# Performance work log

Measured on AMD Instinct MI355X. Metric: run time of the kernel, lower is better.

Reference implementation:

```python
import jax, jax.numpy as jnp
import numpy as np

# Mamba2 hyperparams (mamba_ssm defaults given __init__ args)
D_MODEL = 512
FF = 2048
D_STATE = 128
D_CONV = 4
EXPAND = 2
D_INNER = EXPAND * D_MODEL          # 1024
HEADDIM = 64
NHEADS = D_INNER // HEADDIM         # 16
NGROUPS = 1
CONV_DIM = D_INNER + 2 * NGROUPS * D_STATE       # 1280
D_IN_PROJ = 2 * D_INNER + 2 * NGROUPS * D_STATE + NHEADS  # 2320
CHUNK = 128
EPS = 1e-5


def setup_inputs() -> dict:
    key = jax.random.key(0)
    ks = jax.random.split(key, 16)
    B, S = 8, 2048
    s = 0.02
    dt_init = jax.random.uniform(ks[4], (NHEADS,), minval=0.001, maxval=0.1)
    return {
        # forward args (dropout treated as eval / identity)
        "tgt": jax.random.normal(ks[0], (B, S, D_MODEL), jnp.float32),
        "memory": jax.random.normal(ks[1], (B, 256, D_MODEL), jnp.float32),
        "spatial_shapes": jnp.array([[16, 16]], jnp.int32),
        "level_start_index": jnp.array([0], jnp.int32),
        "valid_ratios": jnp.ones((B, 1, 2), jnp.float32),
        # Mamba2 params
        "in_proj_w": jax.random.normal(ks[2], (D_IN_PROJ, D_MODEL), jnp.float32) * s,
        "conv_w": jax.random.normal(ks[3], (CONV_DIM, D_CONV), jnp.float32) * s,
        "conv_b": jnp.zeros((CONV_DIM,), jnp.float32),
        "dt_bias": jnp.log(jnp.expm1(dt_init)),  # inverse softplus of dt_init
        "A_log": jnp.log(jax.random.uniform(ks[5], (NHEADS,), minval=1.0, maxval=16.0)),
        "D_head": jnp.ones((NHEADS,), jnp.float32),
        "norm_w": jnp.ones((D_INNER,), jnp.float32),
        "out_proj_w": jax.random.normal(ks[6], (D_MODEL, D_INNER), jnp.float32) * s,
        # LayerNorms + FFN
        "norm1_w": jnp.ones((D_MODEL,)), "norm1_b": jnp.zeros((D_MODEL,)),
        "w1": jax.random.normal(ks[7], (FF, D_MODEL), jnp.float32) * s,
        "b1": jnp.zeros((FF,)),
        "w2": jax.random.normal(ks[8], (D_MODEL, FF), jnp.float32) * s,
        "b2": jnp.zeros((D_MODEL,)),
        "norm3_w": jnp.ones((D_MODEL,)), "norm3_b": jnp.zeros((D_MODEL,)),
    }


def _layer_norm(x, w, b):
    m = jnp.mean(x, -1, keepdims=True)
    v = jnp.mean((x - m) ** 2, -1, keepdims=True)
    return (x - m) * jax.lax.rsqrt(v + EPS) * w + b


def _ssd(x, dt, A, Bm, Cm):
    # chunked selective-scan (SSD). x:(b,s,h,p) dt:(b,s,h) A:(h,) Bm,Cm:(b,s,n)
    b, s, h, p = x.shape
    n = Bm.shape[-1]
    c, l = s // CHUNK, CHUNK
    x = x.reshape(b, c, l, h, p)
    dt = dt.reshape(b, c, l, h)
    Bm = Bm.reshape(b, c, l, n)
    Cm = Cm.reshape(b, c, l, n)
    a_cs = jnp.cumsum(dt * A, axis=2)                 # (b,c,l,h) cumulative log-decay
    ac = a_cs.transpose(0, 1, 3, 2)                   # (b,c,h,l)
    mask = jnp.tril(jnp.ones((l, l), bool))
    Lmat = jnp.exp(jnp.where(mask, ac[..., :, None] - ac[..., None, :], -jnp.inf))
    # intra-chunk (causal) contribution
    Y_diag = jnp.einsum('bcin,bcjn,bchij,bcjh,bcjhp->bcihp', Cm, Bm, Lmat, dt, x)
    # per-chunk final states
    decay_end = jnp.exp(a_cs[:, :, -1:, :] - a_cs)    # (b,c,l,h)
    states = jnp.einsum('bcln,bclh,bclh,bclhp->bchpn', Bm, decay_end, dt, x)
    chunk_decay = jnp.exp(a_cs[:, :, -1, :])          # (b,c,h)
    def step(h0, inp):
        cd, st = inp
        return cd[:, :, None, None] * h0 + st, h0
    h_init = jnp.zeros((b, h, p, n), x.dtype)
    _, prev = jax.lax.scan(step, h_init,
                           (chunk_decay.transpose(1, 0, 2),
                            states.transpose(1, 0, 2, 3, 4)))
    prev = prev.transpose(1, 0, 2, 3, 4)              # (b,c,h,p,n) state at chunk start
    Y_off = jnp.einsum('bcln,bchpn,bclh->bclhp', Cm, prev, jnp.exp(a_cs))
    return (Y_diag + Y_off).reshape(b, s, h, p)


def _mamba2(u, in_proj_w, conv_w, conv_b, dt_bias, A_log, D_head, norm_w, out_proj_w):
    Bb, S, _ = u.shape
    zxbcdt = u @ in_proj_w.T                          # (b,s,2320)
    z, xBC, dt = jnp.split(zxbcdt, [D_INNER, D_INNER + CONV_DIM], axis=-1)
    # causal depthwise conv1d + silu
    xp = jnp.pad(xBC, ((0, 0), (D_CONV - 1, 0), (0, 0)))
    conv = sum(xp[:, k:k + S, :] * conv_w[:, k] for k in range(D_CONV)) + conv_b
    xBC = jax.nn.silu(conv)
    x, Bm, Cm = jnp.split(xBC, [D_INNER, D_INNER + NGROUPS * D_STATE], axis=-1)
    dt = jax.nn.softplus(dt + dt_bias)                # (b,s,h)
    A = -jnp.exp(A_log)                               # (h,)
    x = x.reshape(Bb, S, NHEADS, HEADDIM)
    y = _ssd(x, dt, A, Bm, Cm) + D_head[None, None, :, None] * x
    y = y.reshape(Bb, S, D_INNER)
    # gated RMSNorm: rmsnorm(y * silu(z)) * w
    y = y * jax.nn.silu(z)
    y = y * jax.lax.rsqrt(jnp.mean(y * y, -1, keepdims=True) + EPS) * norm_w
    return y @ out_proj_w.T


def reference(tgt, memory, spatial_shapes, level_start_index, valid_ratios,
              in_proj_w, conv_w, conv_b, dt_bias, A_log, D_head, norm_w, out_proj_w,
              norm1_w, norm1_b, w1, b1, w2, b2, norm3_w, norm3_b):
    t2 = _mamba2(tgt, in_proj_w, conv_w, conv_b, dt_bias, A_log, D_head, norm_w, out_proj_w)
    t = _layer_norm(tgt + t2, norm1_w, norm1_b)
    ff = jax.nn.gelu(t @ w1.T + b1, approximate=False) @ w2.T + b2
    return _layer_norm(t + ff, norm3_w, norm3_b)
```

## Files before the change

### kernel.cpp

```cpp
#include <hip/hip_runtime.h>
#include <hip/hip_bf16.h>
#include <math.h>


namespace {
constexpr int BB = 8;
constexpr int S = 2048;
constexpr int DM = 512;
constexpr int DIP = 2320;
constexpr int DIPP = 2432;
constexpr int DI = 1024;
constexpr int CDIM = 1280;
constexpr int NH = 16;
constexpr int HD = 64;
constexpr int DSTATE = 128;
constexpr int CH = 128;
constexpr int NC = S / CH;
constexpr int FF = 2048;
constexpr float EPS = 1e-5f;
constexpr int LP = 132;
}

using bf16_t = __hip_bfloat16;
typedef __attribute__((ext_vector_type(8))) short short8;
typedef __attribute__((ext_vector_type(4))) float f32x4;

__device__ __forceinline__ float gelu_exact(float x) {
    return 0.5f * x * (1.0f + erff(x * 0.7071067811865476f));
}
__device__ __forceinline__ unsigned short f2bfu(float f) {
    bf16_t b = __float2bfloat16(f);
    return *(unsigned short*)&b;
}
__device__ __forceinline__ float bfu2f(unsigned short u) {
    union { unsigned int i; float f; } v; v.i = (unsigned)u << 16; return v.f;
}

__device__ __forceinline__ void block_sum2(float& a, float& b) {
    #pragma unroll
    for (int o = 32; o > 0; o >>= 1) {
        a += __shfl_down(a, o, 64);
        b += __shfl_down(b, o, 64);
    }
    __shared__ float sa[4], sb[4];
    int w = threadIdx.x >> 6;
    if ((threadIdx.x & 63) == 0) { sa[w] = a; sb[w] = b; }
    __syncthreads();
    a = sa[0] + sa[1] + sa[2] + sa[3];
    b = sb[0] + sb[1] + sb[2] + sb[3];
}

template <int BM, int ACT, bool HASBIAS, bool OUTBF>
__global__ __launch_bounds__(256)
void mfma_gemm(const bf16_t* __restrict__ A, const bf16_t* __restrict__ W,
               const float* __restrict__ bias, void* __restrict__ Cout,
               int N, int K, int lda, int ldw, int ldc,
               long batchA, long batchW, long batchC)
{
    A += (long)blockIdx.z * batchA;
    W += (long)blockIdx.z * batchW;
    constexpr int ACH = BM / 64;
    constexpr int NJ = (BM == 128) ? 4 : 2;
    __shared__ bf16_t As[2][BM * 32];
    __shared__ bf16_t Ws[2][4096];
    const int tid = threadIdx.x;
    const int lane = tid & 63;
    const int wave = tid >> 6;
    const long bm = (long)blockIdx.y * BM;
    const int bn = blockIdx.x * 128;

    const int rA = tid & (BM - 1);
    const int qA = tid / BM;
    const int rW = tid & 127;
    const int qW = tid >> 7;
    const bf16_t* Ag = A + (bm + rA) * (long)lda + qA * 8;
    const bf16_t* Wg = W + ((long)bn + rW) * (long)ldw + qW * 8;
    const int laoff0 = (qA * BM + rA) * 8;
    const int laoff1 = ((qA + 2) * BM + rA) * 8;
    const int lwoff0 = (qW * 128 + rW) * 8;
    const int lwoff1 = ((qW + 2) * 128 + rW) * 8;

    const int kq = lane >> 4;
    const int lr = lane & 15;
    const int wm = (BM == 128) ? (wave & 1) * 64 : 0;
    const int wn = (BM == 128) ? (wave >> 1) * 64 : wave * 32;

    f32x4 acc[4][NJ];
    #pragma unroll
    for (int i = 0; i < 4; i++)
        #pragma unroll
        for (int j = 0; j < NJ; j++) acc[i][j] = (f32x4){0.f, 0.f, 0.f, 0.f};

    short8 ra0, ra1, rw0, rw1;
    ra0 = *(const short8*)Ag;
    if (ACH == 2) ra1 = *(const short8*)(Ag + 16);
    rw0 = *(const short8*)Wg;
    rw1 = *(const short8*)(Wg + 16);
    *(short8*)&As[0][laoff0] = ra0;
    if (ACH == 2) *(short8*)&As[0][laoff1] = ra1;
    *(short8*)&Ws[0][lwoff0] = rw0;
    *(short8*)&Ws[0][lwoff1] = rw1;

    const int nt = K / 32;
    for (int t = 0; t < nt; t++) {
        const int cur = t & 1, nxt = cur ^ 1;
        if (t + 1 < nt) {
            const int ko = (t + 1) * 32;
            ra0 = *(const short8*)(Ag + ko);
            if (ACH == 2) ra1 = *(const short8*)(Ag + ko + 16);
            rw0 = *(const short8*)(Wg + ko);
            rw1 = *(const short8*)(Wg + ko + 16);
        }
        __syncthreads();
        short8 af[4], bfr[NJ];
        #pragma unroll
        for (int i = 0; i < 4; i++)
            af[i] = *(const short8*)&As[cur][(kq * BM + wm + i * 16 + lr) * 8];
        #pragma unroll
        for (int j = 0; j < NJ; j++)
            bfr[j] = *(const short8*)&Ws[cur][(kq * 128 + wn + j * 16 + lr) * 8];
        #pragma unroll
        for (int i = 0; i < 4; i++)
            #pragma unroll
            for (int j = 0; j < NJ; j++)
                acc[i][j] = __builtin_amdgcn_mfma_f32_16x16x32_bf16(af[i], bfr[j], acc[i][j], 0, 0, 0);
        if (t + 1 < nt) {
            *(short8*)&As[nxt][laoff0] = ra0;
            if (ACH == 2) *(short8*)&As[nxt][laoff1] = ra1;
            *(short8*)&Ws[nxt][lwoff0] = rw0;
            *(short8*)&Ws[nxt][lwoff1] = rw1;
        }
    }

    #pragma unroll
    for (int i = 0; i < 4; i++) {
        #pragma unroll
        for (int j = 0; j < NJ; j++) {
            int col = bn + wn + j * 16 + lr;
            if (col < N) {
                float bv = HASBIAS ? bias[col] : 0.f;
                #pragma unroll
                for (int r = 0; r < 4; r++) {
                    long row = bm + wm + i * 16 + kq * 4 + r;
                    float v = acc[i][j][r] + bv;
                    if (ACT == 1) v = gelu_exact(v);
                    if (OUTBF) ((bf16_t*)Cout)[row * (long)ldc + col + blockIdx.z * batchC] = __float2bfloat16(v);
                    else       ((float*)Cout)[row * (long)ldc + col + blockIdx.z * batchC] = v;
                }
            }
        }
    }
}

template <int ACT, bool HASBIAS>
__global__ __launch_bounds__(256)
void gemm_kernel(const float* __restrict__ A, const float* __restrict__ W,
                 const float* __restrict__ bias, float* __restrict__ C,
                 int M, int N, int K, int lda, int ldw, int ldc,
                 long batchA, long batchW, long batchC)
{
    A += (long)blockIdx.z * batchA;
    W += (long)blockIdx.z * batchW;
    C += (long)blockIdx.z * batchC;
    __shared__ __align__(16) float Asm[16][68];
    __shared__ __align__(16) float Wsm[16][68];
    const int tid = threadIdx.x;
    const int bm = blockIdx.y * 64;
    const int bn = blockIdx.x * 64;
    const int tm = (tid & 15) * 4;
    const int tn = (tid >> 4) * 4;
    const int lr = tid >> 2;
    const int lk = (tid & 3) * 4;
    const float* Ap = A + (long)(bm + lr) * lda + lk;
    const float* Wp = W + (long)(bn + lr) * ldw + lk;
    const bool wv_ok = (bn + lr) < N;
    float acc[4][4];
    #pragma unroll
    for (int i = 0; i < 4; i++)
        #pragma unroll
        for (int j = 0; j < 4; j++) acc[i][j] = 0.f;

    for (int k0 = 0; k0 < K; k0 += 16) {
        float4 av = *(const float4*)(Ap + k0);
        float4 wv = wv_ok ? *(const float4*)(Wp + k0) : make_float4(0.f, 0.f, 0.f, 0.f);
        Asm[lk + 0][lr] = av.x; Asm[lk + 1][lr] = av.y;
        Asm[lk + 2][lr] = av.z; Asm[lk + 3][lr] = av.w;
        Wsm[lk + 0][lr] = wv.x; Wsm[lk + 1][lr] = wv.y;
        Wsm[lk + 2][lr] = wv.z; Wsm[lk + 3][lr] = wv.w;
        __syncthreads();
        #pragma unroll
        for (int k = 0; k < 16; k++) {
            float4 a = *(const float4*)&Asm[k][tm];
            float4 w = *(const float4*)&Wsm[k][tn];
            acc[0][0] += a.x * w.x; acc[0][1] += a.x * w.y; acc[0][2] += a.x * w.z; acc[0][3] += a.x * w.w;
            acc[1][0] += a.y * w.x; acc[1][1] += a.y * w.y; acc[1][2] += a.y * w.z; acc[1][3] += a.y * w.w;
            acc[2][0] += a.z * w.x; acc[2][1] += a.z * w.y; acc[2][2] += a.z * w.z; acc[2][3] += a.z * w.w;
            acc[3][0] += a.w * w.x; acc[3][1] += a.w * w.y; acc[3][2] += a.w * w.z; acc[3][3] += a.w * w.w;
        }
        __syncthreads();
    }
    #pragma unroll
    for (int i = 0; i < 4; i++) {
        long row = bm + tm + i;
        #pragma unroll
        for (int j = 0; j < 4; j++) {
            int col = bn + tn + j;
            if (col < N) {
                float v = acc[i][j];
                if (HASBIAS) v += bias[col];
                if (ACT == 1) v = gelu_exact(v);
                C[row * ldc + col] = v;
            }
        }
    }
}

__global__ __launch_bounds__(256)
void cvt_bf16(const float* __restrict__ s, bf16_t* __restrict__ d, long n)
{
    long i = ((long)blockIdx.x * 256 + threadIdx.x) * 4;
    if (i >= n) return;
    float4 v = *(const float4*)(s + i);
    d[i + 0] = __float2bfloat16(v.x);
    d[i + 1] = __float2bfloat16(v.y);
    d[i + 2] = __float2bfloat16(v.z);
    d[i + 3] = __float2bfloat16(v.w);
}

__global__ __launch_bounds__(256)
void cvt_bf16_pad(const float* __restrict__ s, bf16_t* __restrict__ d,
                  int rows_src, long total, int cols)
{
    long i = (long)blockIdx.x * 256 + threadIdx.x;
    if (i >= total) return;
    long r = i / cols;
    d[i] = __float2bfloat16(r < rows_src ? s[i] : 0.f);
}

__global__ __launch_bounds__(256)
void conv_silu4(const bf16_t* __restrict__ zx, const float* __restrict__ cw,
                const float* __restrict__ cb, bf16_t* __restrict__ xBC, long count4)
{
    long i4 = (long)blockIdx.x * 256 + threadIdx.x;
    if (i4 >= count4) return;
    long idx = i4 * 4;
    int c = (int)(idx % CDIM);
    long t = idx / CDIM;
    int s = (int)(t % S);
    float v0 = cb[c], v1 = cb[c + 1], v2 = cb[c + 2], v3 = cb[c + 3];
    #pragma unroll
    for (int k = 0; k < 4; k++) {
        int sp = s + k - 3;
        if (sp >= 0) {
            const bf16_t* p = zx + (t + k - 3) * DIP + DI + c;
            unsigned long long u = *(const unsigned long long*)p;
            v0 += bfu2f((unsigned short)(u      )) * cw[(c + 0) * 4 + k];
            v1 += bfu2f((unsigned short)(u >> 16)) * cw[(c + 1) * 4 + k];
            v2 += bfu2f((unsigned short)(u >> 32)) * cw[(c + 2) * 4 + k];
            v3 += bfu2f((unsigned short)(u >> 48)) * cw[(c + 3) * 4 + k];
        }
    }
    v0 = v0 / (1.f + __expf(-v0));
    v1 = v1 / (1.f + __expf(-v1));
    v2 = v2 / (1.f + __expf(-v2));
    v3 = v3 / (1.f + __expf(-v3));
    unsigned long long o = (unsigned long long)f2bfu(v0)
                         | ((unsigned long long)f2bfu(v1) << 16)
                         | ((unsigned long long)f2bfu(v2) << 32)
                         | ((unsigned long long)f2bfu(v3) << 48);
    *(unsigned long long*)&xBC[idx] = o;
}

__global__ __launch_bounds__(256)
void dt_kernel(const float* __restrict__ raw, const float* __restrict__ dt_bias,
               float* __restrict__ dts, long count)
{
    long idx = (long)blockIdx.x * 256 + threadIdx.x;
    if (idx >= count) return;
    float x = raw[idx] + dt_bias[idx & 15];
    dts[idx] = (x > 20.f) ? x : log1pf(__expf(x));
}

__global__ __launch_bounds__(256)
void ssd_states(const bf16_t* __restrict__ xBC, const float* __restrict__ dts,
                const float* __restrict__ A_log,
                float* __restrict__ st, float* __restrict__ acs_all,
                float* __restrict__ cdlog)
{
    const int bid = blockIdx.x;
    const int nh = bid & 1;
    const int h = (bid >> 1) & 15;
    const int c = (bid >> 5) & 15;
    const int b = bid >> 9;
    const int sbid = (b * NC + c) * NH + h;
    const int tid = threadIdx.x;
    const int lane = tid & 63;
    const int wave = tid >> 6;
    __shared__ float dtv[128];
    __shared__ float acs[128];
    __shared__ float wj[128];
    __shared__ bf16_t XT[64 * LP];
    __shared__ bf16_t BwT[64 * LP];
    const long t0 = (long)b * S + (long)c * CH;
    const float Ah = -__expf(A_log[h]);

    if (tid < 128) {
        float d = dts[(t0 + tid) * NH + h];
        dtv[tid] = d;
        acs[tid] = d * Ah;
    }
    __syncthreads();
    for (int off = 1; off < 128; off <<= 1) {
        float add = 0.f;
        if (tid < 128 && tid >= off) add = acs[tid - off];
        __syncthreads();
        if (tid < 128 && tid >= off) acs[tid] += add;
        __syncthreads();
    }
    const float el = acs[127];
    if (tid < 128) wj[tid] = __expf(el - acs[tid]) * dtv[tid];
    if (nh == 0) {
        if (tid < 128) acs_all[(long)sbid * 128 + tid] = acs[tid];
        if (tid == 0) cdlog[sbid] = el;
    }
    __syncthreads();

    const int n0b = nh * 64;
    for (int i = tid; i < 4096; i += 256) {
        int p = i & 63, jp = (i >> 6) << 1;
        unsigned short a = *(const unsigned short*)&xBC[(t0 + jp) * CDIM + h * HD + p];
        unsigned short bb = *(const unsigned short*)&xBC[(t0 + jp + 1) * CDIM + h * HD + p];
        *(unsigned int*)&XT[p * LP + jp] = (unsigned)a | ((unsigned)bb << 16);
    }
    for (int i = tid; i < 4096; i += 256) {
        int n = i & 63, jp = (i >> 6) << 1;
        float v0 = __bfloat162float(xBC[(t0 + jp) * CDIM + DI + n0b + n]) * wj[jp];
        float v1 = __bfloat162float(xBC[(t0 + jp + 1) * CDIM + DI + n0b + n]) * wj[jp + 1];
        *(unsigned int*)&BwT[n * LP + jp] = (unsigned)f2bfu(v0) | ((unsigned)f2bfu(v1) << 16);
    }
    __syncthreads();

    const int kq = lane >> 4;
    const int lr = lane & 15;
    const int p0w = (wave & 1) * 32;
    const int n0w = (wave >> 1) * 32;
    f32x4 acc[2][2];
    #pragma unroll
    for (int i = 0; i < 2; i++)
        #pragma unroll
        for (int j = 0; j < 2; j++) acc[i][j] = (f32x4){0.f, 0.f, 0.f, 0.f};
    #pragma unroll
    for (int t = 0; t < 4; t++) {
        short8 af[2], bfr[2];
        #pragma unroll
        for (int i = 0; i < 2; i++)
            af[i] = *(const short8*)&XT[(p0w + i * 16 + lr) * LP + t * 32 + kq * 8];
        #pragma unroll
        for (int j = 0; j < 2; j++)
            bfr[j] = *(const short8*)&BwT[(n0w + j * 16 + lr) * LP + t * 32 + kq * 8];
        #pragma unroll
        for (int i = 0; i < 2; i++)
            #pragma unroll
            for (int j = 0; j < 2; j++)
                acc[i][j] = __builtin_amdgcn_mfma_f32_16x16x32_bf16(af[i], bfr[j], acc[i][j], 0, 0, 0);
    }
    long base = (long)sbid * 8192;
    #pragma unroll
    for (int i = 0; i < 2; i++)
        #pragma unroll
        for (int j = 0; j < 2; j++) {
            int col = n0b + n0w + j * 16 + lr;
            #pragma unroll
            for (int r = 0; r < 4; r++) {
                int p = p0w + i * 16 + kq * 4 + r;
                st[base + p * 128 + col] = acc[i][j][r];
            }
        }
}

__global__ __launch_bounds__(256)
void ssd_scan(float* __restrict__ st, const float* __restrict__ cdlog)
{
    const int h = blockIdx.x & 15;
    const int b = blockIdx.x >> 4;
    const int q0 = blockIdx.y * 8;
    const int tid = threadIdx.x;
    float prev[8];
    #pragma unroll
    for (int q = 0; q < 8; q++) prev[q] = 0.f;
    for (int c = 0; c < NC; c++) {
        int bc = (b * NC + c) * NH + h;
        float cd = __expf(cdlog[bc]);
        long base = (long)bc * 8192 + (long)q0 * 256;
        #pragma unroll
        for (int q = 0; q < 8; q++) {
            long idx = base + (long)q * 256 + tid;
            float v = st[idx];
            st[idx] = prev[q];
            prev[q] = cd * prev[q] + v;
        }
    }
}

__global__ __launch_bounds__(256)
void ssd_out(const bf16_t* __restrict__ xBC, const float* __restrict__ dts,
             const bf16_t* __restrict__ G, const float* __restrict__ st,
             const float* __restrict__ acs_all, const float* __restrict__ D_head,
             bf16_t* __restrict__ y)
{
    const int bid = blockIdx.x;
    const int ih = bid & 1;
    const int h = (bid >> 1) & 15;
    const int c = (bid >> 5) & 15;
    const int b = bid >> 9;
    const int sbid = (b * NC + c) * NH + h;
    const int tid = threadIdx.x;
    const int lane = tid & 63;
    const int wave = tid >> 6;
    __shared__ float dtv[128];
    __shared__ float acs[128];
    __shared__ float eacs[64];
    __shared__ bf16_t Abuf[64 * LP];
    __shared__ bf16_t Bbuf[64 * LP];
    const long t0 = (long)b * S + (long)c * CH;
    const int m0b = ih * 64;

    if (tid < 128) {
        dtv[tid] = dts[(t0 + tid) * NH + h];
        acs[tid] = acs_all[(long)sbid * 128 + tid];
    }
    __syncthreads();
    if (tid < 64) eacs[tid] = __expf(acs[m0b + tid]);

    const bf16_t* Gb = G + (long)(b * NC + c) * 128 * 128;
    for (int i = tid; i < 4096; i += 256) {
        int rl = i >> 6, kp = (i & 63) << 1;
        int grow = m0b + rl;
        unsigned int g2 = *(const unsigned int*)&Gb[grow * 128 + kp];
        float w0 = (kp     <= grow) ? bfu2f((unsigned short)(g2      )) * __expf(acs[grow] - acs[kp    ]) * dtv[kp    ] : 0.f;
        float w1 = (kp + 1 <= grow) ? bfu2f((unsigned short)(g2 >> 16)) * __expf(acs[grow] - acs[kp + 1]) * dtv[kp + 1] : 0.f;
        *(unsigned int*)&Abuf[rl * LP + kp] = (unsigned)f2bfu(w0) | ((unsigned)f2bfu(w1) << 16);
    }
    for (int i = tid; i < 4096; i += 256) {
        int p = i & 63, jp = (i >> 6) << 1;
        unsigned short a = *(const unsigned short*)&xBC[(t0 + jp) * CDIM + h * HD + p];
        unsigned short bb = *(const unsigned short*)&xBC[(t0 + jp + 1) * CDIM + h * HD + p];
        *(unsigned int*)&Bbuf[p * LP + jp] = (unsigned)a | ((unsigned)bb << 16);
    }
    __syncthreads();

    const int kq = lane >> 4;
    const int lr = lane & 15;
    const int m0w = (wave & 1) * 32;
    const int p0 = (wave >> 1) * 32;
    f32x4 acc[2][2];
    #pragma unroll
    for (int i = 0; i < 2; i++)
        #pragma unroll
        for (int j = 0; j < 2; j++) acc[i][j] = (f32x4){0.f, 0.f, 0.f, 0.f};

    #pragma unroll
    for (int t = 0; t < 4; t++) {
        short8 af[2], bfr[2];
        #pragma unroll
        for (int i = 0; i < 2; i++)
            af[i] = *(const short8*)&Abuf[(m0w + i * 16 + lr) * LP + t * 32 + kq * 8];
        #pragma unroll
        for (int j = 0; j < 2; j++)
            bfr[j] = *(const short8*)&Bbuf[(p0 + j * 16 + lr) * LP + t * 32 + kq * 8];
        #pragma unroll
        for (int i = 0; i < 2; i++)
            #pragma unroll
            for (int j = 0; j < 2; j++)
                acc[i][j] = __builtin_amdgcn_mfma_f32_16x16x32_bf16(af[i], bfr[j], acc[i][j], 0, 0, 0);
    }
    const float Dh = D_head[h];
    float dx[2][2][4];
    #pragma unroll
    for (int i = 0; i < 2; i++)
        #pragma unroll
        for (int j = 0; j < 2; j++) {
            int col = p0 + j * 16 + lr;
            #pragma unroll
            for (int r = 0; r < 4; r++) {
                int rl = m0w + i * 16 + kq * 4 + r;
                dx[i][j][r] = Dh * __bfloat162float(Bbuf[col * LP + m0b + rl]);
            }
        }
    __syncthreads();

    for (int i = tid; i < 4096; i += 256) {
        int rl = i >> 6, np = (i & 63) << 1;
        unsigned int c2 = *(const unsigned int*)&xBC[(t0 + m0b + rl) * CDIM + DI + DSTATE + np];
        float e = eacs[rl];
        float v0 = e * bfu2f((unsigned short)(c2      ));
        float v1 = e * bfu2f((unsigned short)(c2 >> 16));
        *(unsigned int*)&Abuf[rl * LP + np] = (unsigned)f2bfu(v0) | ((unsigned)f2bfu(v1) << 16);
    }
    for (int i = tid; i < 4096; i += 256) {
        int p = i >> 6, np = (i & 63) << 1;
        float2 v = *(const float2*)&st[(long)sbid * 8192 + p * 128 + np];
        *(unsigned int*)&Bbuf[p * LP + np] = (unsigned)f2bfu(v.x) | ((unsigned)f2bfu(v.y) << 16);
    }
    __syncthreads();

    #pragma unroll
    for (int t = 0; t < 4; t++) {
        short8 af[2], bfr[2];
        #pragma unroll
        for (int i = 0; i < 2; i++)
            af[i] = *(const short8*)&Abuf[(m0w + i * 16 + lr) * LP + t * 32 + kq * 8];
        #pragma unroll
        for (int j = 0; j < 2; j++)
            bfr[j] = *(const short8*)&Bbuf[(p0 + j * 16 + lr) * LP + t * 32 + kq * 8];
        #pragma unroll
        for (int i = 0; i < 2; i++)
            #pragma unroll
            for (int j = 0; j < 2; j++)
                acc[i][j] = __builtin_amdgcn_mfma_f32_16x16x32_bf16(af[i], bfr[j], acc[i][j], 0, 0, 0);
    }

    #pragma unroll
    for (int i = 0; i < 2; i++)
        #pragma unroll
        for (int j = 0; j < 2; j++) {
            int col = p0 + j * 16 + lr;
            #pragma unroll
            for (int r = 0; r < 4; r++) {
                int rl = m0w + i * 16 + kq * 4 + r;
                y[(t0 + m0b + rl) * DI + h * HD + col] = __float2bfloat16(acc[i][j][r] + dx[i][j][r]);
            }
        }
}

__global__ __launch_bounds__(256)
void gated_rms(const bf16_t* __restrict__ y, const bf16_t* __restrict__ zx,
               const float* __restrict__ norm_w, bf16_t* __restrict__ yn)
{
    const long t = blockIdx.x;
    const int tid = threadIdx.x;
    float g[4];
    float ss = 0.f, dummy = 0.f;
    #pragma unroll
    for (int q = 0; q < 4; q++) {
        int d = tid + q * 256;
        float zv = __bfloat162float(zx[t * DIP + d]);
        float yv = __bfloat162float(y[t * DI + d]);
        float gv = yv * (zv / (1.f + __expf(-zv)));
        g[q] = gv;
        ss += gv * gv;
    }
    block_sum2(ss, dummy);
    float scale = rsqrtf(ss * (1.f / DI) + EPS);
    #pragma unroll
    for (int q = 0; q < 4; q++) {
        int d = tid + q * 256;
        yn[t * DI + d] = __float2bfloat16(g[q] * scale * norm_w[d]);
    }
}

__global__ __launch_bounds__(256)
void add_ln(const float* __restrict__ x, const float* __restrict__ r,
            const float* __restrict__ w, const float* __restrict__ bpar,
            float* __restrict__ o32, bf16_t* __restrict__ o16)
{
    const long t = blockIdx.x;
    const int tid = threadIdx.x;
    float v[2];
    float s = 0.f, s2 = 0.f;
    #pragma unroll
    for (int q = 0; q < 2; q++) {
        int d = tid + q * 256;
        float vv = x[t * DM + d] + r[t * DM + d];
        v[q] = vv;
        s += vv;
        s2 += vv * vv;
    }
    block_sum2(s, s2);
    float mean = s * (1.f / DM);
    float var = s2 * (1.f / DM) - mean * mean;
    float inv = rsqrtf(var + EPS);
    #pragma unroll
    for (int q = 0; q < 2; q++) {
        int d = tid + q * 256;
        float o = (v[q] - mean) * inv * w[d] + bpar[d];
        o32[t * DM + d] = o;
        o16[t * DM + d] = __float2bfloat16(o);
    }
}


extern "C" void kernel_launch(void* const* d_in, const int* in_sizes, int n_in,
                              void* d_out, int out_size, void* d_ws, size_t ws_size,
                              hipStream_t stream)
{
    const float* tgt       = (const float*)d_in[0];
    const float* in_proj_w = (const float*)d_in[5];
    const float* conv_w    = (const float*)d_in[6];
    const float* conv_b    = (const float*)d_in[7];
    const float* dt_bias   = (const float*)d_in[8];
    const float* A_log     = (const float*)d_in[9];
    const float* D_head    = (const float*)d_in[10];
    const float* norm_w    = (const float*)d_in[11];
    const float* out_proj_w= (const float*)d_in[12];
    const float* norm1_w   = (const float*)d_in[13];
    const float* norm1_b   = (const float*)d_in[14];
    const float* w1        = (const float*)d_in[15];
    const float* b1        = (const float*)d_in[16];
    const float* w2        = (const float*)d_in[17];
    const float* b2        = (const float*)d_in[18];
    const float* norm3_w   = (const float*)d_in[19];
    const float* norm3_b   = (const float*)d_in[20];
    float* out = (float*)d_out;

    float* ws = (float*)d_ws;

    const size_t SZ_INW  = (size_t)DIPP * DM / 2;
    const size_t SZ_OUTW = (size_t)DM * DI / 2;
    const size_t SZ_W1   = (size_t)FF * DM / 2;
    const size_t SZ_W2   = (size_t)DM * FF / 2;
    size_t wo = 0;
    bf16_t* inW  = (bf16_t*)(ws + wo); wo += SZ_INW;
    bf16_t* outW = (bf16_t*)(ws + wo); wo += SZ_OUTW;
    bf16_t* w1b  = (bf16_t*)(ws + wo); wo += SZ_W1;
    bf16_t* w2b  = (bf16_t*)(ws + wo); wo += SZ_W2;
    const size_t WB = wo;

    const size_t PB = (size_t)S * DM / 2
                    + (size_t)S * DIP / 2
                    + (size_t)S * NH
                    + (size_t)S * NH
                    + (size_t)S * CDIM / 2
                    + (size_t)NC * 128 * 128 / 2
                    + (size_t)NC * NH * 128
                    + (size_t)NC * NH
                    + (size_t)S * DI
                    + (size_t)S * DI;
    int NB = 0;
    for (int nb = 8; nb >= 1; nb >>= 1) {
        if (ws_size >= (WB + (size_t)nb * PB) * sizeof(float)) { NB = nb; break; }
    }
    if (NB == 0) return;

    {
        long n = (long)DIPP * DM;
        cvt_bf16_pad<<<(n + 255) / 256, 256, 0, stream>>>(in_proj_w, inW, DIP, n, DM);
        n = (long)DM * DI;
        cvt_bf16<<<(n / 4 + 255) / 256, 256, 0, stream>>>(out_proj_w, outW, n);
        n = (long)FF * DM;
        cvt_bf16<<<(n / 4 + 255) / 256, 256, 0, stream>>>(w1, w1b, n);
        n = (long)DM * FF;
        cvt_bf16<<<(n / 4 + 255) / 256, 256, 0, stream>>>(w2, w2b, n);
    }

    for (int b0 = 0; b0 < BB; b0 += NB) {
        const long Tg = (long)NB * S;
        size_t o = WB;
        bf16_t* tgt_bf = (bf16_t*)(ws + o); o += (size_t)Tg * DM / 2;
        bf16_t* zx     = (bf16_t*)(ws + o); o += (size_t)Tg * DIP / 2;
        float*  dts_raw= ws + o;            o += (size_t)Tg * NH;
        float*  dts    = ws + o;            o += (size_t)Tg * NH;
        bf16_t* xBC    = (bf16_t*)(ws + o); o += (size_t)Tg * CDIM / 2;
        bf16_t* Gbuf   = (bf16_t*)(ws + o); o += (size_t)NB * NC * 128 * 128 / 2;
        float*  acs    = ws + o;            o += (size_t)NB * NC * NH * 128;
        float*  cdl    = ws + o;            o += (size_t)NB * NC * NH;
        float*  ybuf   = ws + o;            o += (size_t)Tg * DI;
        float*  st     = ws + o;            o += (size_t)Tg * DI;

        bf16_t* ybf = (bf16_t*)ybuf;
        bf16_t* yn  = (bf16_t*)st;
        float*  t2  = ybuf;
        float*  tb  = (float*)zx;
        bf16_t* tbb = (bf16_t*)(((float*)zx) + Tg * DM);
        bf16_t* h1  = (bf16_t*)ybuf;
        float*  fb  = (float*)xBC;
        bf16_t* dummy16 = tbb;

        const float* tgt_g = tgt + (long)b0 * S * DM;
        float* out_g = out + (long)b0 * S * DM;

        cvt_bf16<<<((Tg * DM) / 4 + 255) / 256, 256, 0, stream>>>(tgt_g, tgt_bf, Tg * DM);
        mfma_gemm<128, 0, false, true><<<dim3(DIPP / 128, Tg / 128, 1), 256, 0, stream>>>(
            tgt_bf, inW, nullptr, zx, DIP, DM, DM, DM, DIP, 0, 0, 0);
        gemm_kernel<0, false><<<dim3(1, Tg / 64, 1), 256, 0, stream>>>(
            tgt_g, in_proj_w + (long)(DI + CDIM) * DM, nullptr, dts_raw,
            Tg, NH, DM, DM, DM, NH, 0, 0, 0);
        dt_kernel<<<(Tg * NH) / 256, 256, 0, stream>>>(dts_raw, dt_bias, dts, Tg * NH);
        conv_silu4<<<(Tg * CDIM / 4) / 256, 256, 0, stream>>>(zx, conv_w, conv_b, xBC, Tg * CDIM / 4);
        mfma_gemm<128, 0, false, true><<<dim3(1, 1, NB * NC), 256, 0, stream>>>(
            xBC + DI + DSTATE, xBC + DI, nullptr, Gbuf,
            128, DSTATE, CDIM, CDIM, 128,
            (long)CH * CDIM, (long)CH * CDIM, (long)128 * 128);
        ssd_states<<<NB * NC * NH * 2, 256, 0, stream>>>(xBC, dts, A_log, st, acs, cdl);
        ssd_scan<<<dim3(NB * NH, 4), 256, 0, stream>>>(st, cdl);
        ssd_out<<<NB * NC * NH * 2, 256, 0, stream>>>(xBC, dts, Gbuf, st, acs, D_head, ybf);
        gated_rms<<<Tg, 256, 0, stream>>>(ybf, zx, norm_w, yn);
        mfma_gemm<64, 0, false, false><<<dim3(DM / 128, Tg / 64, 1), 256, 0, stream>>>(
            yn, outW, nullptr, t2, DM, DI, DI, DI, DM, 0, 0, 0);
        add_ln<<<Tg, 256, 0, stream>>>(tgt_g, t2, norm1_w, norm1_b, tb, tbb);
        mfma_gemm<128, 1, true, true><<<dim3(FF / 128, Tg / 128, 1), 256, 0, stream>>>(
            tbb, w1b, b1, h1, FF, DM, DM, DM, FF, 0, 0, 0);
        mfma_gemm<64, 0, true, false><<<dim3(DM / 128, Tg / 64, 1), 256, 0, stream>>>(
            h1, w2b, b2, fb, DM, FF, FF, FF, DM, 0, 0, 0);
        add_ln<<<Tg, 256, 0, stream>>>(tb, fb, norm3_w, norm3_b, out_g, dummy16);
    }
}
```

Baseline: 963.2 us.

## Fuse dt softplus into GEMM, tile conv over time, vectorize norm kernels

Softplus and the dt bias move into the small dt GEMM epilogue, which removes the separate dt kernel and its intermediate buffer. The depthwise conv now has each thread handle 16 consecutive timesteps, reusing loaded rows and keeping weights in registers instead of reloading overlapping windows. gated_rms and add_ln switch to vectorized 64/128-bit loads and stores, and add_ln processes two rows per block and skips the unused bf16 write in the final LayerNorm. All are small memory-bound kernels next to the GEMMs and SSD, so the total gain is limited.

```diff
diff --git a/kernel.cpp b/kernel.cpp
--- a/kernel.cpp
+++ b/kernel.cpp
@@ -209,6 +209,7 @@
                 float v = acc[i][j];
                 if (HASBIAS) v += bias[col];
                 if (ACT == 1) v = gelu_exact(v);
+                if (ACT == 2) v = (v > 20.f) ? v : log1pf(__expf(v));
                 C[row * ldc + col] = v;
             }
         }
@@ -238,47 +239,51 @@
 }
 
 __global__ __launch_bounds__(256)
-void conv_silu4(const bf16_t* __restrict__ zx, const float* __restrict__ cw,
-                const float* __restrict__ cb, bf16_t* __restrict__ xBC, long count4)
-{
-    long i4 = (long)blockIdx.x * 256 + threadIdx.x;
-    if (i4 >= count4) return;
-    long idx = i4 * 4;
-    int c = (int)(idx % CDIM);
-    long t = idx / CDIM;
-    int s = (int)(t % S);
-    float v0 = cb[c], v1 = cb[c + 1], v2 = cb[c + 2], v3 = cb[c + 3];
-    #pragma unroll
-    for (int k = 0; k < 4; k++) {
-        int sp = s + k - 3;
-        if (sp >= 0) {
-            const bf16_t* p = zx + (t + k - 3) * DIP + DI + c;
-            unsigned long long u = *(const unsigned long long*)p;
-            v0 += bfu2f((unsigned short)(u      )) * cw[(c + 0) * 4 + k];
-            v1 += bfu2f((unsigned short)(u >> 16)) * cw[(c + 1) * 4 + k];
-            v2 += bfu2f((unsigned short)(u >> 32)) * cw[(c + 2) * 4 + k];
-            v3 += bfu2f((unsigned short)(u >> 48)) * cw[(c + 3) * 4 + k];
-        }
-    }
-    v0 = v0 / (1.f + __expf(-v0));
-    v1 = v1 / (1.f + __expf(-v1));
-    v2 = v2 / (1.f + __expf(-v2));
-    v3 = v3 / (1.f + __expf(-v3));
-    unsigned long long o = (unsigned long long)f2bfu(v0)
-                         | ((unsigned long long)f2bfu(v1) << 16)
-                         | ((unsigned long long)f2bfu(v2) << 32)
-                         | ((unsigned long long)f2bfu(v3) << 48);
-    *(unsigned long long*)&xBC[idx] = o;
-}
-
-__global__ __launch_bounds__(256)
-void dt_kernel(const float* __restrict__ raw, const float* __restrict__ dt_bias,
-               float* __restrict__ dts, long count)
-{
-    long idx = (long)blockIdx.x * 256 + threadIdx.x;
-    if (idx >= count) return;
-    float x = raw[idx] + dt_bias[idx & 15];
-    dts[idx] = (x > 20.f) ? x : log1pf(__expf(x));
+void conv_silu_t16(const bf16_t* __restrict__ zx, const float* __restrict__ cw,
+                   const float* __restrict__ cb, bf16_t* __restrict__ xBC)
+{
+    const int quad = blockIdx.x * 64 + (threadIdx.x & 63);
+    const int wv = threadIdx.x >> 6;
+    const int c = quad * 4;
+    const int s0 = blockIdx.y * 64 + wv * 16;
+    const long t0 = (long)blockIdx.z * S + s0;
+
+    float wgt[4][4];
+    #pragma unroll
+    for (int cc = 0; cc < 4; cc++)
+        #pragma unroll
+        for (int k = 0; k < 4; k++) wgt[cc][k] = cw[(c + cc) * 4 + k];
+    float bias[4];
+    #pragma unroll
+    for (int cc = 0; cc < 4; cc++) bias[cc] = cb[c + cc];
+
+    unsigned long long rows[19];
+    #pragma unroll
+    for (int i = 0; i < 19; i++) {
+        int s = s0 + i - 3;
+        rows[i] = (s >= 0) ? *(const unsigned long long*)&zx[(t0 + i - 3) * DIP + DI + c] : 0ULL;
+    }
+    #pragma unroll
+    for (int i = 0; i < 16; i++) {
+        float v[4];
+        #pragma unroll
+        for (int cc = 0; cc < 4; cc++) v[cc] = bias[cc];
+        #pragma unroll
+        for (int k = 0; k < 4; k++) {
+            unsigned long long u = rows[i + k];
+            v[0] += bfu2f((unsigned short)(u      )) * wgt[0][k];
+            v[1] += bfu2f((unsigned short)(u >> 16)) * wgt[1][k];
+            v[2] += bfu2f((unsigned short)(u >> 32)) * wgt[2][k];
+            v[3] += bfu2f((unsigned short)(u >> 48)) * wgt[3][k];
+        }
+        unsigned long long o = 0;
+        #pragma unroll
+        for (int cc = 0; cc < 4; cc++) {
+            float sv = v[cc] / (1.f + __expf(-v[cc]));
+            o |= (unsigned long long)f2bfu(sv) << (16 * cc);
+        }
+        *(unsigned long long*)&xBC[(t0 + i) * (long)CDIM + c] = o;
+    }
 }
 
 __global__ __launch_bounds__(256)
@@ -538,55 +543,68 @@
                const float* __restrict__ norm_w, bf16_t* __restrict__ yn)
 {
     const long t = blockIdx.x;
-    const int tid = threadIdx.x;
+    const int d = threadIdx.x * 4;
+    unsigned long long zu = *(const unsigned long long*)&zx[t * DIP + d];
+    unsigned long long yu = *(const unsigned long long*)&y[t * DI + d];
     float g[4];
     float ss = 0.f, dummy = 0.f;
     #pragma unroll
     for (int q = 0; q < 4; q++) {
-        int d = tid + q * 256;
-        float zv = __bfloat162float(zx[t * DIP + d]);
-        float yv = __bfloat162float(y[t * DI + d]);
+        float zv = bfu2f((unsigned short)(zu >> (16 * q)));
+        float yv = bfu2f((unsigned short)(yu >> (16 * q)));
         float gv = yv * (zv / (1.f + __expf(-zv)));
         g[q] = gv;
         ss += gv * gv;
     }
     block_sum2(ss, dummy);
     float scale = rsqrtf(ss * (1.f / DI) + EPS);
-    #pragma unroll
-    for (int q = 0; q < 4; q++) {
-        int d = tid + q * 256;
-        yn[t * DI + d] = __float2bfloat16(g[q] * scale * norm_w[d]);
-    }
-}
-
+    unsigned long long o = 0;
+    #pragma unroll
+    for (int q = 0; q < 4; q++)
+        o |= (unsigned long long)f2bfu(g[q] * scale * norm_w[d + q]) << (16 * q);
+    *(unsigned long long*)&yn[t * DI + d] = o;
+}
+
+template <bool W16>
 __global__ __launch_bounds__(256)
 void add_ln(const float* __restrict__ x, const float* __restrict__ r,
             const float* __restrict__ w, const float* __restrict__ bpar,
             float* __restrict__ o32, bf16_t* __restrict__ o16)
 {
-    const long t = blockIdx.x;
     const int tid = threadIdx.x;
-    float v[2];
-    float s = 0.f, s2 = 0.f;
-    #pragma unroll
-    for (int q = 0; q < 2; q++) {
-        int d = tid + q * 256;
-        float vv = x[t * DM + d] + r[t * DM + d];
-        v[q] = vv;
-        s += vv;
-        s2 += vv * vv;
-    }
-    block_sum2(s, s2);
+    const long t = blockIdx.x * 2 + (tid >> 7);
+    const int i = (tid & 127) * 4;
+    float4 xv = *(const float4*)(x + t * DM + i);
+    float4 rv = *(const float4*)(r + t * DM + i);
+    float v[4] = {xv.x + rv.x, xv.y + rv.y, xv.z + rv.z, xv.w + rv.w};
+    float s = v[0] + v[1] + v[2] + v[3];
+    float s2 = v[0]*v[0] + v[1]*v[1] + v[2]*v[2] + v[3]*v[3];
+    #pragma unroll
+    for (int o = 32; o > 0; o >>= 1) {
+        s += __shfl_down(s, o, 64);
+        s2 += __shfl_down(s2, o, 64);
+    }
+    __shared__ float sa[4], sb[4];
+    int wv = tid >> 6;
+    if ((tid & 63) == 0) { sa[wv] = s; sb[wv] = s2; }
+    __syncthreads();
+    int base = (tid >> 7) * 2;
+    s = sa[base] + sa[base + 1];
+    s2 = sb[base] + sb[base + 1];
     float mean = s * (1.f / DM);
     float var = s2 * (1.f / DM) - mean * mean;
     float inv = rsqrtf(var + EPS);
-    #pragma unroll
-    for (int q = 0; q < 2; q++) {
-        int d = tid + q * 256;
-        float o = (v[q] - mean) * inv * w[d] + bpar[d];
-        o32[t * DM + d] = o;
-        o16[t * DM + d] = __float2bfloat16(o);
-    }
+    float4 ov;
+    float* op = (float*)&ov;
+    unsigned long long o16u = 0;
+    #pragma unroll
+    for (int q = 0; q < 4; q++) {
+        float o = (v[q] - mean) * inv * w[i + q] + bpar[i + q];
+        op[q] = o;
+        if (W16) o16u |= (unsigned long long)f2bfu(o) << (16 * q);
+    }
+    *(float4*)(o32 + t * DM + i) = ov;
+    if (W16) *(unsigned long long*)&o16[t * DM + i] = o16u;
 }
 
 
@@ -629,7 +647,6 @@
     const size_t PB = (size_t)S * DM / 2
                     + (size_t)S * DIP / 2
                     + (size_t)S * NH
-                    + (size_t)S * NH
                     + (size_t)S * CDIM / 2
                     + (size_t)NC * 128 * 128 / 2
                     + (size_t)NC * NH * 128
@@ -658,7 +675,6 @@
         size_t o = WB;
         bf16_t* tgt_bf = (bf16_t*)(ws + o); o += (size_t)Tg * DM / 2;
         bf16_t* zx     = (bf16_t*)(ws + o); o += (size_t)Tg * DIP / 2;
-        float*  dts_raw= ws + o;            o += (size_t)Tg * NH;
         float*  dts    = ws + o;            o += (size_t)Tg * NH;
         bf16_t* xBC    = (bf16_t*)(ws + o); o += (size_t)Tg * CDIM / 2;
         bf16_t* Gbuf   = (bf16_t*)(ws + o); o += (size_t)NB * NC * 128 * 128 / 2;
@@ -674,7 +690,6 @@
         bf16_t* tbb = (bf16_t*)(((float*)zx) + Tg * DM);
         bf16_t* h1  = (bf16_t*)ybuf;
         float*  fb  = (float*)xBC;
-        bf16_t* dummy16 = tbb;
 
         const float* tgt_g = tgt + (long)b0 * S * DM;
         float* out_g = out + (long)b0 * S * DM;
@@ -682,11 +697,10 @@
         cvt_bf16<<<((Tg * DM) / 4 + 255) / 256, 256, 0, stream>>>(tgt_g, tgt_bf, Tg * DM);
         mfma_gemm<128, 0, false, true><<<dim3(DIPP / 128, Tg / 128, 1), 256, 0, stream>>>(
             tgt_bf, inW, nullptr, zx, DIP, DM, DM, DM, DIP, 0, 0, 0);
-        gemm_kernel<0, false><<<dim3(1, Tg / 64, 1), 256, 0, stream>>>(
-            tgt_g, in_proj_w + (long)(DI + CDIM) * DM, nullptr, dts_raw,
+        gemm_kernel<2, true><<<dim3(1, Tg / 64, 1), 256, 0, stream>>>(
+            tgt_g, in_proj_w + (long)(DI + CDIM) * DM, dt_bias, dts,
             Tg, NH, DM, DM, DM, NH, 0, 0, 0);
-        dt_kernel<<<(Tg * NH) / 256, 256, 0, stream>>>(dts_raw, dt_bias, dts, Tg * NH);
-        conv_silu4<<<(Tg * CDIM / 4) / 256, 256, 0, stream>>>(zx, conv_w, conv_b, xBC, Tg * CDIM / 4);
+        conv_silu_t16<<<dim3(CDIM / 256, S / 64, NB), 256, 0, stream>>>(zx, conv_w, conv_b, xBC);
         mfma_gemm<128, 0, false, true><<<dim3(1, 1, NB * NC), 256, 0, stream>>>(
             xBC + DI + DSTATE, xBC + DI, nullptr, Gbuf,
             128, DSTATE, CDIM, CDIM, 128,
@@ -697,11 +711,11 @@
         gated_rms<<<Tg, 256, 0, stream>>>(ybf, zx, norm_w, yn);
         mfma_gemm<64, 0, false, false><<<dim3(DM / 128, Tg / 64, 1), 256, 0, stream>>>(
             yn, outW, nullptr, t2, DM, DI, DI, DI, DM, 0, 0, 0);
-        add_ln<<<Tg, 256, 0, stream>>>(tgt_g, t2, norm1_w, norm1_b, tb, tbb);
+        add_ln<true><<<Tg / 2, 256, 0, stream>>>(tgt_g, t2, norm1_w, norm1_b, tb, tbb);
         mfma_gemm<128, 1, true, true><<<dim3(FF / 128, Tg / 128, 1), 256, 0, stream>>>(
             tbb, w1b, b1, h1, FF, DM, DM, DM, FF, 0, 0, 0);
         mfma_gemm<64, 0, true, false><<<dim3(DM / 128, Tg / 64, 1), 256, 0, stream>>>(
             h1, w2b, b2, fb, DM, FF, FF, FF, DM, 0, 0, 0);
-        add_ln<<<Tg, 256, 0, stream>>>(tb, fb, norm3_w, norm3_b, out_g, dummy16);
-    }
-}
+        add_ln<false><<<Tg / 2, 256, 0, stream>>>(tb, fb, norm3_w, norm3_b, out_g, nullptr);
+    }
+}
```

Measured after the change: 839.1 us. -12.9%, faster.
